# Optimization experiments

Hardware: AMD Instinct MI355X
Metric: run time of the kernel (lower is better)

Reference implementation:

```python
import jax, jax.numpy as jnp
import numpy as np

N0, N1, N2 = 120000, 30000, 6000   # node frontier sizes per hop
E0, E1 = 480000, 96000             # sampled edges per layer (~fanout 16)
D = 128                            # in_channels == hidden_size
R = 8                              # num_relations
NB = 4                             # num_bases
ETOT = 3000000                     # global edge count (edge_type_all)


def setup_inputs() -> dict:
    key = jax.random.key(0)
    ks = jax.random.split(key, 24)
    s = 1.0 / np.sqrt(D)
    f32 = jnp.float32
    inp = {
        "x": jax.random.normal(ks[0], (N0, D), dtype=f32),
        "src0": jax.random.randint(ks[1], (E0,), 0, N0),
        "dst0": jax.random.randint(ks[2], (E0,), 0, N1),
        "e_id0": jax.random.randint(ks[3], (E0,), 0, ETOT),
        "src1": jax.random.randint(ks[4], (E1,), 0, N1),
        "dst1": jax.random.randint(ks[5], (E1,), 0, N2),
        "e_id1": jax.random.randint(ks[6], (E1,), 0, ETOT),
        "edge_type_all": jax.random.randint(ks[7], (ETOT,), 0, R),
        # pre_layer: linear + relu
        "pre_W": jax.random.normal(ks[8], (D, D), dtype=f32) * s,
        "pre_b": jnp.zeros((D,), f32),
        # RGCNConv layer 0 (basis decomposition)
        "basis0": jax.random.normal(ks[9], (NB, D, D), dtype=f32) * s,
        "comp0": jax.random.normal(ks[10], (R, NB), dtype=f32) * (1.0 / np.sqrt(NB)),
        "root0": jax.random.normal(ks[11], (D, D), dtype=f32) * s,
        "bias0": jnp.zeros((D,), f32),
        "g0": jnp.ones((D,), f32),
        "be0": jnp.zeros((D,), f32),
        # RGCNConv layer 1
        "basis1": jax.random.normal(ks[12], (NB, D, D), dtype=f32) * s,
        "comp1": jax.random.normal(ks[13], (R, NB), dtype=f32) * (1.0 / np.sqrt(NB)),
        "root1": jax.random.normal(ks[14], (D, D), dtype=f32) * s,
        "bias1": jnp.zeros((D,), f32),
        "g1": jnp.ones((D,), f32),
        "be1": jnp.zeros((D,), f32),
        # post_layer: single linear
        "post_W": jax.random.normal(ks[15], (D, D), dtype=f32) * s,
        "post_b": jnp.zeros((D,), f32),
    }
    return inp


def _layernorm(x, g, b, eps=1e-5):
    mu = jnp.mean(x, axis=-1, keepdims=True)
    var = jnp.mean(jnp.square(x - mu), axis=-1, keepdims=True)
    return (x - mu) * jax.lax.rsqrt(var + eps) * g + b


def _rgcn_conv(x, n_dst, src, dst, etype, basis, comp, root, bias):
    # Bipartite RGCNConv with basis decomposition and mean aggregation.
    # Since messages W[r] @ x[src] are linear, aggregate per relation first
    # (segment_sum of raw features), then apply the relation weight once.
    x_t = x[:n_dst]                                    # [n_dst, D]
    out = x_t @ root + bias                            # root/self transform
    W = jnp.einsum('rb,bio->rio', comp, basis)         # [R, D, D]
    x_j = x[src]                                       # [E, D] gather
    deg = jax.ops.segment_sum(jnp.ones(src.shape[0], x.dtype), dst,
                              num_segments=n_dst)      # mean over all relations
    agg = jnp.zeros((n_dst, W.shape[-1]), x.dtype)
    for r in range(W.shape[0]):                        # R=8 structurally distinct
        m = (etype == r).astype(x.dtype)[:, None]
        s_r = jax.ops.segment_sum(x_j * m, dst, num_segments=n_dst)
        agg = agg + s_r @ W[r]
    return out + agg / jnp.maximum(deg, 1.0)[:, None]


def reference(x, src0, dst0, e_id0, src1, dst1, e_id1, edge_type_all,
              pre_W, pre_b, basis0, comp0, root0, bias0, g0, be0,
              basis1, comp1, root1, bias1, g1, be1, post_W, post_b):
    # pre_layer: linear + relu (GeneralMultiLayer, final_act=True)
    h = jax.nn.relu(x @ pre_W + pre_b)
    # layer 0: edge-type gather -> relational conv -> norm -> act (eval: no dropout)
    h = _rgcn_conv(h, N1, src0, dst0, edge_type_all[e_id0],
                   basis0, comp0, root0, bias0)
    h = jax.nn.relu(_layernorm(h, g0, be0))
    # layer 1
    h = _rgcn_conv(h, N2, src1, dst1, edge_type_all[e_id1],
                   basis1, comp1, root1, bias1)
    h = jax.nn.relu(_layernorm(h, g1, be1))
    # post_layer: single linear MLP
    return h @ post_W + post_b
```

## Files before the change

### kernel.cpp

```cpp
#include <hip/hip_runtime.h>
#include <cstdint>

#define DD 128
#define CAP 64
#define E0C 480000
#define E1C 96000
#define N0C 120000
#define N1C 30000
#define N2C 6000

typedef unsigned short u16;
typedef __attribute__((ext_vector_type(8))) short bf16x8;
typedef __attribute__((ext_vector_type(16))) float f32x16;

__device__ __forceinline__ u16 f2b(float f) {
    union { float f; unsigned u; } a; a.f = f;
    unsigned r = (a.u + 0x7fffu + ((a.u >> 16) & 1u)) >> 16;
    return (u16)r;
}
__device__ __forceinline__ float b2f(u16 u) {
    union { unsigned u; float f; } a; a.u = ((unsigned)u) << 16;
    return a.f;
}

struct WtJob { const float* src[12]; };
__global__ __launch_bounds__(256) void prep_kernel(
    WtJob job, u16* __restrict__ dst, int* __restrict__ cnt0, int* __restrict__ cnt1)
{
    int gtid = blockIdx.x * 256 + threadIdx.x;
    for (int i = gtid; i < N1C + N2C; i += 256 * 256) {
        if (i < N1C) cnt0[i] = 0; else cnt1[i - N1C] = 0;
    }
    if (blockIdx.x >= 192) return;
    __shared__ float tile[32][33];
    int m = blockIdx.x >> 4;
    int t4 = blockIdx.x & 15;
    int tr = (t4 >> 2) * 32;
    int tc = (t4 & 3) * 32;
    int lx = threadIdx.x & 31, ly = threadIdx.x >> 5;
    #pragma unroll
    for (int yy = 0; yy < 32; yy += 8)
        tile[ly + yy][lx] = job.src[m][(tr + ly + yy) * DD + tc + lx];
    __syncthreads();
    int tid = threadIdx.x;
    if (tid < 128) {
        int nl = tid >> 2, kch = tid & 3;
        int k = tr + kch * 8, n = tc + nl;
        int kc = k >> 4, half = (k >> 3) & 1;
        int t = n >> 5, l31 = n & 31;
        bf16x8 pk;
        #pragma unroll
        for (int j = 0; j < 8; ++j) pk[j] = (short)f2b(tile[kch * 8 + j][nl]);
        *(bf16x8*)(dst + (size_t)m * 16384 + kc * 2048 + t * 512 + half * 256 + l31 * 8) = pk;
    }
}

__global__ __launch_bounds__(256) void pre_fill_kernel(
    const float* __restrict__ x,
    const int* __restrict__ src0, const int* __restrict__ dst0, const int* __restrict__ eid0,
    const int* __restrict__ src1, const int* __restrict__ dst1, const int* __restrict__ eid1,
    const int* __restrict__ etype,
    int* __restrict__ cnt0, int* __restrict__ cnt1,
    int* __restrict__ ep0, int* __restrict__ ep1,
    const u16* __restrict__ Wr, const float* __restrict__ bias,
    u16* __restrict__ h0)
{
    int gtid = blockIdx.x * 256 + threadIdx.x;
    int nthr = gridDim.x * 256;
    for (int e = gtid; e < E0C + E1C; e += nthr) {
        bool L0 = e < E0C;
        int ee = L0 ? e : e - E0C;
        int d   = L0 ? dst0[ee] : dst1[ee];
        int eid = L0 ? eid0[ee] : eid1[ee];
        int s   = L0 ? src0[ee] : src1[ee];
        int r = etype[eid];
        int* cnt = L0 ? cnt0 : cnt1;
        int* ep  = L0 ? ep0  : ep1;
        int pos = atomicAdd(&cnt[d], 1);
        if (pos < CAP) ep[(size_t)d * CAP + pos] = s | (r << 28);
    }

    int wave = threadIdx.x >> 6;
    int lane = threadIdx.x & 63;
    int l31 = lane & 31, half = lane >> 5;
    int ntile = (N0C + 31) >> 5;
    for (int tile = blockIdx.x * 4 + wave; tile < ntile; tile += gridDim.x * 4) {
        int m0 = tile * 32;
        int arow = m0 + l31;
        bool rv = arow < N0C;
        f32x16 acc[4];
        #pragma unroll
        for (int t = 0; t < 4; ++t)
            #pragma unroll
            for (int i = 0; i < 16; ++i) acc[t][i] = 0.f;

        const float* Aq = x + (size_t)arow * DD;
        float4 st[16];
        if (rv) {
            #pragma unroll
            for (int c = 0; c < 16; ++c)
                st[c] = *(const float4*)(Aq + ((c >> 1) * 16 + half * 8) + (c & 1) * 4);
        } else {
            #pragma unroll
            for (int c = 0; c < 16; ++c) st[c] = make_float4(0.f, 0.f, 0.f, 0.f);
        }
        #pragma unroll
        for (int kc = 0; kc < 8; ++kc) {
            bf16x8 bfr[4];
            #pragma unroll
            for (int t = 0; t < 4; ++t)
                bfr[t] = *(const bf16x8*)(Wr + (size_t)((kc * 4 + t) * 64 + lane) * 8);
            float4 u0 = st[2 * kc], u1 = st[2 * kc + 1];
            bf16x8 af;
            af[0] = (short)f2b(u0.x); af[1] = (short)f2b(u0.y);
            af[2] = (short)f2b(u0.z); af[3] = (short)f2b(u0.w);
            af[4] = (short)f2b(u1.x); af[5] = (short)f2b(u1.y);
            af[6] = (short)f2b(u1.z); af[7] = (short)f2b(u1.w);
            #pragma unroll
            for (int t = 0; t < 4; ++t)
                acc[t] = __builtin_amdgcn_mfma_f32_32x32x16_bf16(af, bfr[t], acc[t], 0, 0, 0);
        }

        float bb[4];
        #pragma unroll
        for (int t = 0; t < 4; ++t) bb[t] = bias[t * 32 + l31];
        #pragma unroll
        for (int reg = 0; reg < 16; ++reg) {
            int rl = (reg & 3) + 8 * (reg >> 2) + 4 * half;
            int row = m0 + rl;
            if (row < N0C) {
                #pragma unroll
                for (int t = 0; t < 4; ++t)
                    ((u16*)h0)[(size_t)row * DD + t * 32 + l31] =
                        f2b(fmaxf(acc[t][reg] + bb[t], 0.f));
            }
        }
    }
}

__global__ __launch_bounds__(256) void agg_kernel(
    const u16* __restrict__ h, const int* __restrict__ cnt,
    const int* __restrict__ ep, const float* __restrict__ comp,
    u16* __restrict__ T, int ndst)
{
    __shared__ float4 cmp4[8];
    if (threadIdx.x < 8) cmp4[threadIdx.x] = ((const float4*)comp)[threadIdx.x];
    __syncthreads();
    int row = blockIdx.x * 4 + (threadIdx.x >> 6);
    if (row >= ndst) return;
    int lane = threadIdx.x & 63;
    int n = cnt[row];
    int end = n < CAP ? n : CAP;
    const int* erow = ep + (size_t)row * CAP;
    float a0[4] = {0.f, 0.f, 0.f, 0.f};
    float a1[4] = {0.f, 0.f, 0.f, 0.f};
    int j = 0;
    for (; j + 8 <= end; j += 8) {
        int vv[8]; unsigned gg[8];
        #pragma unroll
        for (int u = 0; u < 8; ++u) vv[u] = erow[j + u];
        #pragma unroll
        for (int u = 0; u < 8; ++u)
            gg[u] = *(const unsigned*)(h + (size_t)(vv[u] & 0x0FFFFFFF) * DD + 2 * lane);
        #pragma unroll
        for (int u = 0; u < 8; ++u) {
            float4 c = cmp4[vv[u] >> 28];
            float x0 = b2f((u16)(gg[u] & 0xffffu));
            float x1 = b2f((u16)(gg[u] >> 16));
            a0[0] = fmaf(c.x, x0, a0[0]); a1[0] = fmaf(c.x, x1, a1[0]);
            a0[1] = fmaf(c.y, x0, a0[1]); a1[1] = fmaf(c.y, x1, a1[1]);
            a0[2] = fmaf(c.z, x0, a0[2]); a1[2] = fmaf(c.z, x1, a1[2]);
            a0[3] = fmaf(c.w, x0, a0[3]); a1[3] = fmaf(c.w, x1, a1[3]);
        }
    }
    for (; j < end; ++j) {
        int v = erow[j];
        unsigned g = *(const unsigned*)(h + (size_t)(v & 0x0FFFFFFF) * DD + 2 * lane);
        float4 c = cmp4[v >> 28];
        float x0 = b2f((u16)(g & 0xffffu));
        float x1 = b2f((u16)(g >> 16));
        a0[0] = fmaf(c.x, x0, a0[0]); a1[0] = fmaf(c.x, x1, a1[0]);
        a0[1] = fmaf(c.y, x0, a0[1]); a1[1] = fmaf(c.y, x1, a1[1]);
        a0[2] = fmaf(c.z, x0, a0[2]); a1[2] = fmaf(c.z, x1, a1[2]);
        a0[3] = fmaf(c.w, x0, a0[3]); a1[3] = fmaf(c.w, x1, a1[3]);
    }
    float inv = 1.f / fmaxf((float)n, 1.f);
    #pragma unroll
    for (int b = 0; b < 4; ++b) {
        unsigned pk = (unsigned)f2b(a0[b] * inv) | ((unsigned)f2b(a1[b] * inv) << 16);
        *(unsigned*)(T + ((size_t)b * ndst + row) * DD + 2 * lane) = pk;
    }
}

template<int WPB, bool OBF16, bool LN>
__global__ __launch_bounds__(WPB * 64) void mfma_gemm(
    const u16* __restrict__ Ap, int nplanes, const u16* __restrict__ Ar,
    const u16* __restrict__ Wp, const u16* __restrict__ Wr,
    const float* __restrict__ bias, const float* __restrict__ gw,
    const float* __restrict__ bw, void* __restrict__ Cv, int nrows)
{
    int wave = threadIdx.x >> 6;
    int lane = threadIdx.x & 63;
    int l31 = lane & 31, half = lane >> 5;
    int m0 = (blockIdx.x * WPB + wave) * 32;
    int arow = m0 + l31;
    bool rv = arow < nrows;
    f32x16 acc[4];
    #pragma unroll
    for (int t = 0; t < 4; ++t)
        #pragma unroll
        for (int i = 0; i < 16; ++i) acc[t][i] = 0.f;

    bf16x8 A0[8], A1[8];
    {
        const u16* Ainit = (nplanes == 0) ? Ar : Ap;
        if (rv) {
            #pragma unroll
            for (int c = 0; c < 8; ++c)
                A0[c] = *(const bf16x8*)(Ainit + (size_t)arow * DD + c * 16 + half * 8);
        } else {
            #pragma unroll
            for (int c = 0; c < 8; ++c) A0[c] = (bf16x8){0,0,0,0,0,0,0,0};
        }
    }
    for (int p = 0; p <= nplanes; ++p) {
        const u16* Wsel = (p == nplanes) ? Wr : Wp + p * 16384;
        if (p < nplanes) {
            const u16* An = (p + 1 == nplanes) ? Ar : Ap + (size_t)(p + 1) * nrows * DD;
            if (rv) {
                #pragma unroll
                for (int c = 0; c < 8; ++c)
                    A1[c] = *(const bf16x8*)(An + (size_t)arow * DD + c * 16 + half * 8);
            } else {
                #pragma unroll
                for (int c = 0; c < 8; ++c) A1[c] = (bf16x8){0,0,0,0,0,0,0,0};
            }
        }
        #pragma unroll
        for (int kc = 0; kc < 8; ++kc) {
            bf16x8 bfr[4];
            #pragma unroll
            for (int t = 0; t < 4; ++t)
                bfr[t] = *(const bf16x8*)(Wsel + (size_t)((kc * 4 + t) * 64 + lane) * 8);
            #pragma unroll
            for (int t = 0; t < 4; ++t)
                acc[t] = __builtin_amdgcn_mfma_f32_32x32x16_bf16(A0[kc], bfr[t], acc[t], 0, 0, 0);
        }
        if (p < nplanes) {
            #pragma unroll
            for (int c = 0; c < 8; ++c) A0[c] = A1[c];
        }
    }

    float bb[4];
    #pragma unroll
    for (int t = 0; t < 4; ++t) bb[t] = bias[t * 32 + l31];
    float gg[4], ww[4];
    if (LN) {
        #pragma unroll
        for (int t = 0; t < 4; ++t) { gg[t] = gw[t * 32 + l31]; ww[t] = bw[t * 32 + l31]; }
    }

    #pragma unroll
    for (int reg = 0; reg < 16; ++reg) {
        int rl = (reg & 3) + 8 * (reg >> 2) + 4 * half;
        int row = m0 + rl;
        float v[4];
        #pragma unroll
        for (int t = 0; t < 4; ++t) v[t] = acc[t][reg] + bb[t];
        if (LN) {
            float s1 = 0.f, s2 = 0.f;
            #pragma unroll
            for (int t = 0; t < 4; ++t) { s1 += v[t]; s2 += v[t] * v[t]; }
            #pragma unroll
            for (int o = 1; o < 32; o <<= 1) {
                s1 += __shfl_xor(s1, o);
                s2 += __shfl_xor(s2, o);
            }
            float mu = s1 * (1.f / 128.f);
            float var = s2 * (1.f / 128.f) - mu * mu;
            float rstd = rsqrtf(fmaxf(var, 0.f) + 1e-5f);
            #pragma unroll
            for (int t = 0; t < 4; ++t)
                v[t] = fmaxf((v[t] - mu) * rstd * gg[t] + ww[t], 0.f);
        }
        if (row < nrows) {
            #pragma unroll
            for (int t = 0; t < 4; ++t) {
                if (OBF16) ((u16*)Cv)[(size_t)row * DD + t * 32 + l31] = f2b(v[t]);
                else       ((float*)Cv)[(size_t)row * DD + t * 32 + l31] = v[t];
            }
        }
    }
}

extern "C" void kernel_launch(void* const* d_in, const int* in_sizes, int n_in,
                              void* d_out, int out_size, void* d_ws, size_t ws_size,
                              hipStream_t stream)
{
    const float* x     = (const float*)d_in[0];
    const int* src0    = (const int*)d_in[1];
    const int* dst0    = (const int*)d_in[2];
    const int* eid0    = (const int*)d_in[3];
    const int* src1    = (const int*)d_in[4];
    const int* dst1    = (const int*)d_in[5];
    const int* eid1    = (const int*)d_in[6];
    const int* etype   = (const int*)d_in[7];
    const float* preW  = (const float*)d_in[8];
    const float* preb  = (const float*)d_in[9];
    const float* basis0 = (const float*)d_in[10];
    const float* comp0  = (const float*)d_in[11];
    const float* root0  = (const float*)d_in[12];
    const float* bias0  = (const float*)d_in[13];
    const float* g0    = (const float*)d_in[14];
    const float* be0   = (const float*)d_in[15];
    const float* basis1 = (const float*)d_in[16];
    const float* comp1  = (const float*)d_in[17];
    const float* root1  = (const float*)d_in[18];
    const float* bias1  = (const float*)d_in[19];
    const float* g1    = (const float*)d_in[20];
    const float* be1   = (const float*)d_in[21];
    const float* postW = (const float*)d_in[22];
    const float* postb = (const float*)d_in[23];
    float* out = (float*)d_out;

    char* ws = (char*)d_ws;
    size_t o = 0;
    auto alloc = [&](size_t bytes) { char* p = ws + o; o += (bytes + 255) & ~(size_t)255; return p; };
    u16* h0   = (u16*)alloc((size_t)N0C * DD * 2);
    u16* T0   = (u16*)alloc((size_t)4 * N1C * DD * 2);
    u16* h1   = (u16*)alloc((size_t)N1C * DD * 2);
    u16* T1   = (u16*)alloc((size_t)4 * N2C * DD * 2);
    u16* h2   = (u16*)alloc((size_t)N2C * DD * 2);
    u16* wt   = (u16*)alloc((size_t)12 * 16384 * 2);
    int* cnt0 = (int*)alloc((size_t)N1C * 4);
    int* cnt1 = (int*)alloc((size_t)N2C * 4);
    int* ep0  = (int*)alloc((size_t)N1C * CAP * 4);
    int* ep1  = (int*)alloc((size_t)N2C * CAP * 4);

    WtJob job;
    job.src[0] = preW;
    for (int b = 0; b < 4; ++b) job.src[1 + b] = basis0 + (size_t)b * 16384;
    job.src[5] = root0;
    for (int b = 0; b < 4; ++b) job.src[6 + b] = basis1 + (size_t)b * 16384;
    job.src[10] = root1;
    job.src[11] = postW;

    prep_kernel<<<256, 256, 0, stream>>>(job, wt, cnt0, cnt1);
    pre_fill_kernel<<<(N0C + 127) / 128, 256, 0, stream>>>(
        x, src0, dst0, eid0, src1, dst1, eid1, etype,
        cnt0, cnt1, ep0, ep1, wt + 0 * 16384, preb, h0);
    agg_kernel<<<(N1C + 3) / 4, 256, 0, stream>>>(h0, cnt0, ep0, comp0, T0, N1C);
    mfma_gemm<1, true, true><<<(N1C + 31) / 32, 64, 0, stream>>>(
        T0, 4, h0, wt + 1 * 16384, wt + 5 * 16384, bias0, g0, be0, h1, N1C);
    agg_kernel<<<(N2C + 3) / 4, 256, 0, stream>>>(h1, cnt1, ep1, comp1, T1, N2C);
    mfma_gemm<1, true, true><<<(N2C + 31) / 32, 64, 0, stream>>>(
        T1, 4, h1, wt + 6 * 16384, wt + 10 * 16384, bias1, g1, be1, h2, N2C);
    mfma_gemm<1, false, false><<<(N2C + 31) / 32, 64, 0, stream>>>(
        nullptr, 0, h2, nullptr, wt + 11 * 16384, postb, nullptr, nullptr, out, N2C);
}
```

Baseline: 297.2 us.

## Fuse aggregation, relational GEMM, layernorm and post linear into per-layer kernels

Merges the edge aggregation and the basis/root GEMM with layernorm into one kernel per layer. Aggregated basis planes now stay in LDS instead of making a round trip through global T buffers. The post linear is fused into the second layer's kernel, and the GEMM work is split across 4 waves by output column with a cross-wave LDS reduction for layernorm. This removes three launches and the T/h2 global traffic. In exchange, each block serializes 8 rows of gather per wave before its GEMM can start, and the gather unroll grows from 8 to 16 edges.

```diff
diff --git a/kernel.cpp b/kernel.cpp
--- a/kernel.cpp
+++ b/kernel.cpp
@@ -3,6 +3,7 @@
 
 #define DD 128
 #define CAP 64
+#define LSTR 132
 #define E0C 480000
 #define E1C 96000
 #define N0C 120000
@@ -21,6 +22,12 @@
 __device__ __forceinline__ float b2f(u16 u) {
     union { unsigned u; float f; } a; a.u = ((unsigned)u) << 16;
     return a.f;
+}
+__device__ __forceinline__ bf16x8 ldsfrag(const u16* p) {
+    union { uint2 u2[2]; bf16x8 v; } u;
+    u.u2[0] = *(const uint2*)p;
+    u.u2[1] = *(const uint2*)(p + 4);
+    return u.v;
 }
 
 struct WtJob { const float* src[12]; };
@@ -88,11 +95,9 @@
         int m0 = tile * 32;
         int arow = m0 + l31;
         bool rv = arow < N0C;
-        f32x16 acc[4];
-        #pragma unroll
-        for (int t = 0; t < 4; ++t)
-            #pragma unroll
-            for (int i = 0; i < 16; ++i) acc[t][i] = 0.f;
+        f32x16 acc;
+        #pragma unroll
+        for (int i = 0; i < 16; ++i) acc[i] = 0.f;
 
         const float* Aq = x + (size_t)arow * DD;
         float4 st[16];
@@ -104,6 +109,11 @@
             #pragma unroll
             for (int c = 0; c < 16; ++c) st[c] = make_float4(0.f, 0.f, 0.f, 0.f);
         }
+        f32x16 accs[4];
+        #pragma unroll
+        for (int t = 0; t < 4; ++t)
+            #pragma unroll
+            for (int i = 0; i < 16; ++i) accs[t][i] = 0.f;
         #pragma unroll
         for (int kc = 0; kc < 8; ++kc) {
             bf16x8 bfr[4];
@@ -118,9 +128,8 @@
             af[6] = (short)f2b(u1.z); af[7] = (short)f2b(u1.w);
             #pragma unroll
             for (int t = 0; t < 4; ++t)
-                acc[t] = __builtin_amdgcn_mfma_f32_32x32x16_bf16(af, bfr[t], acc[t], 0, 0, 0);
-        }
-
+                accs[t] = __builtin_amdgcn_mfma_f32_32x32x16_bf16(af, bfr[t], accs[t], 0, 0, 0);
+        }
         float bb[4];
         #pragma unroll
         for (int t = 0; t < 4; ++t) bb[t] = bias[t * 32 + l31];
@@ -131,165 +140,167 @@
             if (row < N0C) {
                 #pragma unroll
                 for (int t = 0; t < 4; ++t)
-                    ((u16*)h0)[(size_t)row * DD + t * 32 + l31] =
-                        f2b(fmaxf(acc[t][reg] + bb[t], 0.f));
+                    h0[(size_t)row * DD + t * 32 + l31] =
+                        f2b(fmaxf(accs[t][reg] + bb[t], 0.f));
             }
         }
     }
 }
 
-__global__ __launch_bounds__(256) void agg_kernel(
+template<bool POST>
+__global__ __launch_bounds__(256) void layer_kernel(
     const u16* __restrict__ h, const int* __restrict__ cnt,
     const int* __restrict__ ep, const float* __restrict__ comp,
-    u16* __restrict__ T, int ndst)
-{
-    __shared__ float4 cmp4[8];
-    if (threadIdx.x < 8) cmp4[threadIdx.x] = ((const float4*)comp)[threadIdx.x];
-    __syncthreads();
-    int row = blockIdx.x * 4 + (threadIdx.x >> 6);
-    if (row >= ndst) return;
-    int lane = threadIdx.x & 63;
-    int n = cnt[row];
-    int end = n < CAP ? n : CAP;
-    const int* erow = ep + (size_t)row * CAP;
-    float a0[4] = {0.f, 0.f, 0.f, 0.f};
-    float a1[4] = {0.f, 0.f, 0.f, 0.f};
-    int j = 0;
-    for (; j + 8 <= end; j += 8) {
-        int vv[8]; unsigned gg[8];
-        #pragma unroll
-        for (int u = 0; u < 8; ++u) vv[u] = erow[j + u];
-        #pragma unroll
-        for (int u = 0; u < 8; ++u)
-            gg[u] = *(const unsigned*)(h + (size_t)(vv[u] & 0x0FFFFFFF) * DD + 2 * lane);
-        #pragma unroll
-        for (int u = 0; u < 8; ++u) {
-            float4 c = cmp4[vv[u] >> 28];
-            float x0 = b2f((u16)(gg[u] & 0xffffu));
-            float x1 = b2f((u16)(gg[u] >> 16));
-            a0[0] = fmaf(c.x, x0, a0[0]); a1[0] = fmaf(c.x, x1, a1[0]);
-            a0[1] = fmaf(c.y, x0, a0[1]); a1[1] = fmaf(c.y, x1, a1[1]);
-            a0[2] = fmaf(c.z, x0, a0[2]); a1[2] = fmaf(c.z, x1, a1[2]);
-            a0[3] = fmaf(c.w, x0, a0[3]); a1[3] = fmaf(c.w, x1, a1[3]);
-        }
-    }
-    for (; j < end; ++j) {
-        int v = erow[j];
-        unsigned g = *(const unsigned*)(h + (size_t)(v & 0x0FFFFFFF) * DD + 2 * lane);
-        float4 c = cmp4[v >> 28];
-        float x0 = b2f((u16)(g & 0xffffu));
-        float x1 = b2f((u16)(g >> 16));
-        a0[0] = fmaf(c.x, x0, a0[0]); a1[0] = fmaf(c.x, x1, a1[0]);
-        a0[1] = fmaf(c.y, x0, a0[1]); a1[1] = fmaf(c.y, x1, a1[1]);
-        a0[2] = fmaf(c.z, x0, a0[2]); a1[2] = fmaf(c.z, x1, a1[2]);
-        a0[3] = fmaf(c.w, x0, a0[3]); a1[3] = fmaf(c.w, x1, a1[3]);
-    }
-    float inv = 1.f / fmaxf((float)n, 1.f);
-    #pragma unroll
-    for (int b = 0; b < 4; ++b) {
-        unsigned pk = (unsigned)f2b(a0[b] * inv) | ((unsigned)f2b(a1[b] * inv) << 16);
-        *(unsigned*)(T + ((size_t)b * ndst + row) * DD + 2 * lane) = pk;
-    }
-}
-
-template<int WPB, bool OBF16, bool LN>
-__global__ __launch_bounds__(WPB * 64) void mfma_gemm(
-    const u16* __restrict__ Ap, int nplanes, const u16* __restrict__ Ar,
     const u16* __restrict__ Wp, const u16* __restrict__ Wr,
     const float* __restrict__ bias, const float* __restrict__ gw,
-    const float* __restrict__ bw, void* __restrict__ Cv, int nrows)
+    const float* __restrict__ bw,
+    const u16* __restrict__ Wpost, const float* __restrict__ postb,
+    u16* __restrict__ hout, float* __restrict__ out, int ndst)
 {
-    int wave = threadIdx.x >> 6;
-    int lane = threadIdx.x & 63;
-    int l31 = lane & 31, half = lane >> 5;
-    int m0 = (blockIdx.x * WPB + wave) * 32;
+    __shared__ u16 Tt[4 * 32 * LSTR];
+    __shared__ float2 lnb[32][4];
+    __shared__ float4 cmp4[8];
+    int tid = threadIdx.x;
+    int wv = tid >> 6, lane = tid & 63, l31 = lane & 31, half = lane >> 5;
+    int m0 = blockIdx.x * 32;
+    if (tid < 8) cmp4[tid] = ((const float4*)comp)[tid];
+    __syncthreads();
+
+    for (int i = 0; i < 8; ++i) {
+        int lr = wv * 8 + i;
+        int row = m0 + lr;
+        float a0[4] = {0.f, 0.f, 0.f, 0.f};
+        float a1[4] = {0.f, 0.f, 0.f, 0.f};
+        float inv = 1.f;
+        if (row < ndst) {
+            int n = cnt[row];
+            int end = n < CAP ? n : CAP;
+            const int* erow = ep + (size_t)row * CAP;
+            int j = 0;
+            for (; j + 16 <= end; j += 16) {
+                int vv[16]; unsigned gg[16];
+                #pragma unroll
+                for (int u = 0; u < 16; ++u) vv[u] = erow[j + u];
+                #pragma unroll
+                for (int u = 0; u < 16; ++u)
+                    gg[u] = *(const unsigned*)(h + (size_t)(vv[u] & 0x0FFFFFFF) * DD + 2 * lane);
+                #pragma unroll
+                for (int u = 0; u < 16; ++u) {
+                    float4 c = cmp4[vv[u] >> 28];
+                    float x0 = b2f((u16)(gg[u] & 0xffffu));
+                    float x1 = b2f((u16)(gg[u] >> 16));
+                    a0[0] = fmaf(c.x, x0, a0[0]); a1[0] = fmaf(c.x, x1, a1[0]);
+                    a0[1] = fmaf(c.y, x0, a0[1]); a1[1] = fmaf(c.y, x1, a1[1]);
+                    a0[2] = fmaf(c.z, x0, a0[2]); a1[2] = fmaf(c.z, x1, a1[2]);
+                    a0[3] = fmaf(c.w, x0, a0[3]); a1[3] = fmaf(c.w, x1, a1[3]);
+                }
+            }
+            for (; j < end; ++j) {
+                int v = erow[j];
+                unsigned g = *(const unsigned*)(h + (size_t)(v & 0x0FFFFFFF) * DD + 2 * lane);
+                float4 c = cmp4[v >> 28];
+                float x0 = b2f((u16)(g & 0xffffu));
+                float x1 = b2f((u16)(g >> 16));
+                a0[0] = fmaf(c.x, x0, a0[0]); a1[0] = fmaf(c.x, x1, a1[0]);
+                a0[1] = fmaf(c.y, x0, a0[1]); a1[1] = fmaf(c.y, x1, a1[1]);
+                a0[2] = fmaf(c.z, x0, a0[2]); a1[2] = fmaf(c.z, x1, a1[2]);
+                a0[3] = fmaf(c.w, x0, a0[3]); a1[3] = fmaf(c.w, x1, a1[3]);
+            }
+            inv = 1.f / fmaxf((float)n, 1.f);
+        }
+        #pragma unroll
+        for (int b = 0; b < 4; ++b) {
+            unsigned pk = (unsigned)f2b(a0[b] * inv) | ((unsigned)f2b(a1[b] * inv) << 16);
+            *(unsigned*)&Tt[(size_t)(b * 32 + lr) * LSTR + 2 * lane] = pk;
+        }
+    }
+
     int arow = m0 + l31;
-    bool rv = arow < nrows;
-    f32x16 acc[4];
-    #pragma unroll
-    for (int t = 0; t < 4; ++t)
-        #pragma unroll
-        for (int i = 0; i < 16; ++i) acc[t][i] = 0.f;
-
-    bf16x8 A0[8], A1[8];
-    {
-        const u16* Ainit = (nplanes == 0) ? Ar : Ap;
-        if (rv) {
-            #pragma unroll
-            for (int c = 0; c < 8; ++c)
-                A0[c] = *(const bf16x8*)(Ainit + (size_t)arow * DD + c * 16 + half * 8);
-        } else {
-            #pragma unroll
-            for (int c = 0; c < 8; ++c) A0[c] = (bf16x8){0,0,0,0,0,0,0,0};
-        }
-    }
-    for (int p = 0; p <= nplanes; ++p) {
-        const u16* Wsel = (p == nplanes) ? Wr : Wp + p * 16384;
-        if (p < nplanes) {
-            const u16* An = (p + 1 == nplanes) ? Ar : Ap + (size_t)(p + 1) * nrows * DD;
-            if (rv) {
-                #pragma unroll
-                for (int c = 0; c < 8; ++c)
-                    A1[c] = *(const bf16x8*)(An + (size_t)arow * DD + c * 16 + half * 8);
-            } else {
-                #pragma unroll
-                for (int c = 0; c < 8; ++c) A1[c] = (bf16x8){0,0,0,0,0,0,0,0};
-            }
-        }
+    bool rv = arow < ndst;
+    bf16x8 R[8];
+    if (rv) {
+        #pragma unroll
+        for (int c = 0; c < 8; ++c)
+            R[c] = *(const bf16x8*)(h + (size_t)arow * DD + c * 16 + half * 8);
+    } else {
+        #pragma unroll
+        for (int c = 0; c < 8; ++c) R[c] = (bf16x8){0,0,0,0,0,0,0,0};
+    }
+    __syncthreads();
+
+    f32x16 acc;
+    #pragma unroll
+    for (int i = 0; i < 16; ++i) acc[i] = 0.f;
+    for (int p = 0; p < 4; ++p) {
         #pragma unroll
         for (int kc = 0; kc < 8; ++kc) {
-            bf16x8 bfr[4];
-            #pragma unroll
-            for (int t = 0; t < 4; ++t)
-                bfr[t] = *(const bf16x8*)(Wsel + (size_t)((kc * 4 + t) * 64 + lane) * 8);
-            #pragma unroll
-            for (int t = 0; t < 4; ++t)
-                acc[t] = __builtin_amdgcn_mfma_f32_32x32x16_bf16(A0[kc], bfr[t], acc[t], 0, 0, 0);
-        }
-        if (p < nplanes) {
-            #pragma unroll
-            for (int c = 0; c < 8; ++c) A0[c] = A1[c];
-        }
-    }
-
-    float bb[4];
-    #pragma unroll
-    for (int t = 0; t < 4; ++t) bb[t] = bias[t * 32 + l31];
-    float gg[4], ww[4];
-    if (LN) {
-        #pragma unroll
-        for (int t = 0; t < 4; ++t) { gg[t] = gw[t * 32 + l31]; ww[t] = bw[t * 32 + l31]; }
-    }
-
+            bf16x8 af = ldsfrag(&Tt[(size_t)(p * 32 + l31) * LSTR + kc * 16 + half * 8]);
+            bf16x8 bf = *(const bf16x8*)(Wp + (size_t)p * 16384 + ((kc * 4 + wv) * 64 + lane) * 8);
+            acc = __builtin_amdgcn_mfma_f32_32x32x16_bf16(af, bf, acc, 0, 0, 0);
+        }
+    }
+    #pragma unroll
+    for (int kc = 0; kc < 8; ++kc) {
+        bf16x8 bf = *(const bf16x8*)(Wr + ((kc * 4 + wv) * 64 + lane) * 8);
+        acc = __builtin_amdgcn_mfma_f32_32x32x16_bf16(R[kc], bf, acc, 0, 0, 0);
+    }
+
+    float bb = bias[wv * 32 + l31];
+    float G = gw[wv * 32 + l31];
+    float Bt = bw[wv * 32 + l31];
+    float v[16];
+    #pragma unroll
+    for (int reg = 0; reg < 16; ++reg) v[reg] = acc[reg] + bb;
+    #pragma unroll
+    for (int reg = 0; reg < 16; ++reg) {
+        float s1 = v[reg], s2 = v[reg] * v[reg];
+        #pragma unroll
+        for (int o = 1; o < 32; o <<= 1) {
+            s1 += __shfl_xor(s1, o);
+            s2 += __shfl_xor(s2, o);
+        }
+        if (l31 == 0) {
+            int rl = (reg & 3) + 8 * (reg >> 2) + 4 * half;
+            lnb[rl][wv] = make_float2(s1, s2);
+        }
+    }
+    __syncthreads();
     #pragma unroll
     for (int reg = 0; reg < 16; ++reg) {
         int rl = (reg & 3) + 8 * (reg >> 2) + 4 * half;
+        float2 t0 = lnb[rl][0], t1 = lnb[rl][1], t2 = lnb[rl][2], t3 = lnb[rl][3];
+        float s1 = t0.x + t1.x + t2.x + t3.x;
+        float s2 = t0.y + t1.y + t2.y + t3.y;
+        float mu = s1 * (1.f / 128.f);
+        float var = s2 * (1.f / 128.f) - mu * mu;
+        float rstd = rsqrtf(fmaxf(var, 0.f) + 1e-5f);
+        float y = fmaxf((v[reg] - mu) * rstd * G + Bt, 0.f);
         int row = m0 + rl;
-        float v[4];
-        #pragma unroll
-        for (int t = 0; t < 4; ++t) v[t] = acc[t][reg] + bb[t];
-        if (LN) {
-            float s1 = 0.f, s2 = 0.f;
-            #pragma unroll
-            for (int t = 0; t < 4; ++t) { s1 += v[t]; s2 += v[t] * v[t]; }
-            #pragma unroll
-            for (int o = 1; o < 32; o <<= 1) {
-                s1 += __shfl_xor(s1, o);
-                s2 += __shfl_xor(s2, o);
-            }
-            float mu = s1 * (1.f / 128.f);
-            float var = s2 * (1.f / 128.f) - mu * mu;
-            float rstd = rsqrtf(fmaxf(var, 0.f) + 1e-5f);
-            #pragma unroll
-            for (int t = 0; t < 4; ++t)
-                v[t] = fmaxf((v[t] - mu) * rstd * gg[t] + ww[t], 0.f);
-        }
-        if (row < nrows) {
-            #pragma unroll
-            for (int t = 0; t < 4; ++t) {
-                if (OBF16) ((u16*)Cv)[(size_t)row * DD + t * 32 + l31] = f2b(v[t]);
-                else       ((float*)Cv)[(size_t)row * DD + t * 32 + l31] = v[t];
-            }
+        if (POST) {
+            Tt[(size_t)rl * LSTR + wv * 32 + l31] = f2b(y);
+        } else if (row < ndst) {
+            hout[(size_t)row * DD + wv * 32 + l31] = f2b(y);
+        }
+    }
+
+    if (POST) {
+        __syncthreads();
+        f32x16 a2;
+        #pragma unroll
+        for (int i = 0; i < 16; ++i) a2[i] = 0.f;
+        #pragma unroll
+        for (int kc = 0; kc < 8; ++kc) {
+            bf16x8 af = ldsfrag(&Tt[(size_t)l31 * LSTR + kc * 16 + half * 8]);
+            bf16x8 bf = *(const bf16x8*)(Wpost + ((kc * 4 + wv) * 64 + lane) * 8);
+            a2 = __builtin_amdgcn_mfma_f32_32x32x16_bf16(af, bf, a2, 0, 0, 0);
+        }
+        float pb = postb[wv * 32 + l31];
+        #pragma unroll
+        for (int reg = 0; reg < 16; ++reg) {
+            int rl = (reg & 3) + 8 * (reg >> 2) + 4 * half;
+            int row = m0 + rl;
+            if (row < ndst)
+                out[(size_t)row * DD + wv * 32 + l31] = a2[reg] + pb;
         }
     }
 }
@@ -328,10 +339,7 @@
     size_t o = 0;
     auto alloc = [&](size_t bytes) { char* p = ws + o; o += (bytes + 255) & ~(size_t)255; return p; };
     u16* h0   = (u16*)alloc((size_t)N0C * DD * 2);
-    u16* T0   = (u16*)alloc((size_t)4 * N1C * DD * 2);
     u16* h1   = (u16*)alloc((size_t)N1C * DD * 2);
-    u16* T1   = (u16*)alloc((size_t)4 * N2C * DD * 2);
-    u16* h2   = (u16*)alloc((size_t)N2C * DD * 2);
     u16* wt   = (u16*)alloc((size_t)12 * 16384 * 2);
     int* cnt0 = (int*)alloc((size_t)N1C * 4);
     int* cnt1 = (int*)alloc((size_t)N2C * 4);
@@ -350,12 +358,10 @@
     pre_fill_kernel<<<(N0C + 127) / 128, 256, 0, stream>>>(
         x, src0, dst0, eid0, src1, dst1, eid1, etype,
         cnt0, cnt1, ep0, ep1, wt + 0 * 16384, preb, h0);
-    agg_kernel<<<(N1C + 3) / 4, 256, 0, stream>>>(h0, cnt0, ep0, comp0, T0, N1C);
-    mfma_gemm<1, true, true><<<(N1C + 31) / 32, 64, 0, stream>>>(
-        T0, 4, h0, wt + 1 * 16384, wt + 5 * 16384, bias0, g0, be0, h1, N1C);
-    agg_kernel<<<(N2C + 3) / 4, 256, 0, stream>>>(h1, cnt1, ep1, comp1, T1, N2C);
-    mfma_gemm<1, true, true><<<(N2C + 31) / 32, 64, 0, stream>>>(
-        T1, 4, h1, wt + 6 * 16384, wt + 10 * 16384, bias1, g1, be1, h2, N2C);
-    mfma_gemm<1, false, false><<<(N2C + 31) / 32, 64, 0, stream>>>(
-        nullptr, 0, h2, nullptr, wt + 11 * 16384, postb, nullptr, nullptr, out, N2C);
-}
+    layer_kernel<false><<<(N1C + 31) / 32, 256, 0, stream>>>(
+        h0, cnt0, ep0, comp0, wt + 1 * 16384, wt + 5 * 16384,
+        bias0, g0, be0, nullptr, nullptr, h1, nullptr, N1C);
+    layer_kernel<true><<<(N2C + 31) / 32, 256, 0, stream>>>(
+        h1, cnt1, ep1, comp1, wt + 6 * 16384, wt + 10 * 16384,
+        bias1, g1, be1, wt + 11 * 16384, postb, nullptr, out, N2C);
+}
```

New measurement: 364.2 us. +22.5%, slower.
